# Optimization experiments

Hardware: AMD Instinct MI355X
Metric: run time of the kernel (lower is better)

## Reference

```python
import jax, jax.numpy as jnp
import numpy as np

NPAT, NCON, E, H, L = 50000, 20000, 800000, 128, 2
DP, DC = 64, 128
N = NPAT + NCON  # homogeneous node count


def setup_inputs() -> dict:
    key = jax.random.key(0)
    k = jax.random.split(key, 12)
    s = 0.05
    return {
        "x_patient": jax.random.normal(k[0], (NPAT, DP), jnp.float32),
        "x_concept": jax.random.normal(k[1], (NCON, DC), jnp.float32),
        "W_p": jax.random.normal(k[2], (DP, H), jnp.float32) * s,
        "b_p": jnp.zeros((H,), jnp.float32),
        "W_c": jax.random.normal(k[3], (DC, H), jnp.float32) * s,
        "b_c": jnp.zeros((H,), jnp.float32),
        "W_root": jax.random.normal(k[4], (L, H, H), jnp.float32) * s,
        "b_root": jnp.zeros((L, H), jnp.float32),
        "W_rel": jax.random.normal(k[5], (L, 2, H, H), jnp.float32) * s,
        "src_pc": jax.random.randint(k[6], (E,), 0, NPAT),
        "dst_pc": jax.random.randint(k[7], (E,), 0, NCON),
        "src_cp": jax.random.randint(k[8], (E,), 0, NCON),
        "dst_cp": jax.random.randint(k[9], (E,), 0, NPAT),
    }


def reference(x_patient, x_concept, W_p, b_p, W_c, b_c, W_root, b_root, W_rel,
              src_pc, dst_pc, src_cp, dst_cp):
    # per-node-type linear projection, then concat into homogeneous graph
    # (patient offset 0, concept offset NPAT)
    x = jnp.concatenate([x_patient @ W_p + b_p, x_concept @ W_c + b_c], axis=0)  # [N, H]
    rel_edges = [(src_pc, dst_pc + NPAT), (src_cp + NPAT, dst_cp)]
    ones = jnp.ones((E,), jnp.float32)
    # per-relation in-degree for mean aggregation (zero-deg nodes -> 0 output)
    counts = [jnp.maximum(jax.ops.segment_sum(ones, d, num_segments=N), 1.0)[:, None]
              for _, d in rel_edges]
    for l in range(L):
        out = x @ W_root[l] + b_root[l]  # root transform + bias
        for r, (src, dst) in enumerate(rel_edges):
            msg = x[src] @ W_rel[l, r]  # [E, H] gather + relation transform
            out = out + jax.ops.segment_sum(msg, dst, num_segments=N) / counts[r]
        x = jax.nn.relu(out)
    return x  # [N, H]; rows [0:NPAT] are patient embeddings, rest concepts
```

## Files before the change

### kernel.cpp

```cpp
#include <hip/hip_runtime.h>
#include <hip/hip_bf16.h>

#define NPAT 50000
#define NCON 20000
#define NN   70000
#define EE   800000
#define H    128

#define NCON_AL  20032
#define SEGN     (NCON_AL + NPAT)
#define NBUCK    1095
#define RELSPLIT_B 313
#define BUCKCAP  5120
#define SUBS     16
#define SUBCAP   (BUCKCAP / SUBS)
#define BPE      4096
#define NBB      ((2 * EE + BPE - 1) / BPE)
#define CAP      4096

typedef __attribute__((ext_vector_type(8))) short bf16x8;
typedef __attribute__((ext_vector_type(4))) float f32x4;

__device__ inline unsigned short f2bf(float f) {
    unsigned u = __float_as_uint(f);
    unsigned r = (u + 0x7FFFu + ((u >> 16) & 1u)) >> 16;
    return (unsigned short)r;
}
__device__ inline float bf2f_lo(unsigned v) { return __uint_as_float(v << 16); }
__device__ inline float bf2f_hi(unsigned v) { return __uint_as_float(v & 0xFFFF0000u); }

__global__ void init_gcur_kernel(int* __restrict__ gcur) {
    int j = blockIdx.x * 256 + threadIdx.x;
    if (j < NBUCK * SUBS) gcur[j] = (j >> 4) * BUCKCAP + (j & (SUBS - 1)) * SUBCAP;
}

__global__ __launch_bounds__(512) void binpack_kernel(
        const int* __restrict__ dst_pc, const int* __restrict__ src_pc,
        const int* __restrict__ dst_cp, const int* __restrict__ src_cp,
        int* __restrict__ gcur, unsigned* __restrict__ pairs) {
    __shared__ unsigned sval[BPE];
    __shared__ unsigned short sbkt[BPE];
    __shared__ int cnt[NBUCK];
    __shared__ int delta[NBUCK];
    __shared__ int partial[512];
    int t = threadIdx.x, blk = blockIdx.x;
    int base = blk * BPE;
    int n = min(BPE, 2 * EE - base);

    for (int i = t; i < NBUCK; i += 512) cnt[i] = 0;
    __syncthreads();

    unsigned pay[8];
    int bkt[8];
#pragma unroll
    for (int q = 0; q < 8; q++) {
        int li = q * 512 + t;
        bkt[q] = -1;
        if (li < n) {
            int i = base + li;
            int seg, src;
            if (i < EE) { seg = dst_pc[i];                src = src_pc[i]; }
            else        { seg = NCON_AL + dst_cp[i - EE]; src = src_cp[i - EE]; }
            int b = seg >> 6;
            pay[q] = (unsigned)src | ((unsigned)(seg & 63) << 16);
            bkt[q] = b;
            atomicAdd(&cnt[b], 1);
        }
    }
    __syncthreads();

    const int PER = (NBUCK + 511) / 512;
    int beg = t * PER;
    int s = 0;
#pragma unroll
    for (int k = 0; k < PER; k++) { int i = beg + k; if (i < NBUCK) s += cnt[i]; }
    partial[t] = s;
    __syncthreads();
    for (int o = 1; o < 512; o <<= 1) {
        int v = (t >= o) ? partial[t - o] : 0;
        __syncthreads();
        partial[t] += v;
        __syncthreads();
    }
    int run = partial[t] - s;
    int sub = blk & (SUBS - 1);
    int prefk[PER];
#pragma unroll
    for (int k = 0; k < PER; k++) {
        int i = beg + k;
        if (i < NBUCK) {
            prefk[k] = run;
            int c = cnt[i];
            if (c > 0) {
                int gb = atomicAdd(&gcur[i * SUBS + sub], c);
                delta[i] = gb - run;
            }
            run += c;
        }
    }
    __syncthreads();
#pragma unroll
    for (int k = 0; k < PER; k++) { int i = beg + k; if (i < NBUCK) cnt[i] = prefk[k]; }
    __syncthreads();

#pragma unroll
    for (int q = 0; q < 8; q++) {
        if (bkt[q] >= 0) {
            int b = bkt[q];
            int pos = atomicAdd(&cnt[b], 1);
            sval[pos] = pay[q];
            sbkt[pos] = (unsigned short)b;
        }
    }
    __syncthreads();
    for (int i = t; i < n; i += 512)
        pairs[delta[sbkt[i]] + i] = sval[i];
}

__global__ __launch_bounds__(512) void aggregate_kernel(
        const unsigned short* __restrict__ xbf, const unsigned* __restrict__ pairs,
        const int* __restrict__ gcur, unsigned short* __restrict__ aggn) {
    __shared__ int cnt64[64];
    __shared__ int soff[65];
    __shared__ int scur[64];
    __shared__ unsigned short ssrc[CAP];
    int t = threadIdx.x, b = blockIdx.x;
    if (t < 64) cnt64[t] = 0;
    __syncthreads();
    for (int s = 0; s < SUBS; s++) {
        int rbase = b * BUCKCAP + s * SUBCAP;
        int rcnt = gcur[b * SUBS + s] - rbase;
        for (int i = t; i < rcnt; i += 512)
            atomicAdd(&cnt64[pairs[rbase + i] >> 16], 1);
    }
    __syncthreads();
    if (t < 64) {
        int v = cnt64[t];
        int s = v;
#pragma unroll
        for (int o = 1; o < 64; o <<= 1) {
            int u = __shfl_up(s, o);
            if (t >= o) s += u;
        }
        soff[t + 1] = s;
        if (t == 0) soff[0] = 0;
        scur[t] = s - v;
    }
    __syncthreads();
    for (int s = 0; s < SUBS; s++) {
        int rbase = b * BUCKCAP + s * SUBCAP;
        int rcnt = gcur[b * SUBS + s] - rbase;
        for (int i = t; i < rcnt; i += 512) {
            unsigned p = pairs[rbase + i];
            int pos = atomicAdd(&scur[p >> 16], 1);
            ssrc[pos] = (unsigned short)(p & 0xFFFF);
        }
    }
    __syncthreads();
    int wv = t >> 6, lane = t & 63;
    int h = lane >> 5, cl = lane & 31;
    int rowbase = (b < RELSPLIT_B) ? 0 : NPAT;
    int seglim  = (b < RELSPLIT_B) ? NCON : SEGN;
    const unsigned* xw = (const unsigned*)xbf;
    for (int i = 0; i < 8; i++) {
        int d = wv * 8 + i;
        int seg = b * 64 + d;
        if (seg >= seglim) continue;
        int beg = soff[d], end = soff[d + 1];
        float4 a0 = {0.f, 0.f, 0.f, 0.f}, a1 = {0.f, 0.f, 0.f, 0.f};
        int j = beg;
        if ((end - beg) & 1) {
            int s0 = ssrc[j];
            uint2 v = *(const uint2*)&xw[(size_t)(rowbase + s0) * 64 + 2 * cl];
            if (h == 0) {
                a0.x += bf2f_lo(v.x); a0.y += bf2f_hi(v.x);
                a0.z += bf2f_lo(v.y); a0.w += bf2f_hi(v.y);
            }
            j++;
        }
        for (; j + 3 < end; j += 4) {
            int sA = ssrc[j + h];
            int sB = ssrc[j + 2 + h];
            uint2 vA = *(const uint2*)&xw[(size_t)(rowbase + sA) * 64 + 2 * cl];
            uint2 vB = *(const uint2*)&xw[(size_t)(rowbase + sB) * 64 + 2 * cl];
            a0.x += bf2f_lo(vA.x); a0.y += bf2f_hi(vA.x);
            a0.z += bf2f_lo(vA.y); a0.w += bf2f_hi(vA.y);
            a1.x += bf2f_lo(vB.x); a1.y += bf2f_hi(vB.x);
            a1.z += bf2f_lo(vB.y); a1.w += bf2f_hi(vB.y);
        }
        if (j + 1 < end) {
            int sA = ssrc[j + h];
            uint2 vA = *(const uint2*)&xw[(size_t)(rowbase + sA) * 64 + 2 * cl];
            a0.x += bf2f_lo(vA.x); a0.y += bf2f_hi(vA.x);
            a0.z += bf2f_lo(vA.y); a0.w += bf2f_hi(vA.y);
        }
        a0.x += a1.x; a0.y += a1.y; a0.z += a1.z; a0.w += a1.w;
        a0.x += __shfl_xor(a0.x, 32);
        a0.y += __shfl_xor(a0.y, 32);
        a0.z += __shfl_xor(a0.z, 32);
        a0.w += __shfl_xor(a0.w, 32);
        if (h == 0) {
            float inv = 1.0f / (float)max(end - beg, 1);
            ushort4 o;
            o.x = f2bf(a0.x * inv); o.y = f2bf(a0.y * inv);
            o.z = f2bf(a0.z * inv); o.w = f2bf(a0.w * inv);
            *(ushort4*)&aggn[(size_t)seg * H + 4 * cl] = o;
        }
    }
}

#define BM 128
#define BK 8

struct GemmJob {
    const float* A1;
    const float* B1;
    const float* bias; unsigned short* Cbf;
    int lda1, K1, M;
};

__global__ void gemm_dual_kernel(GemmJob j0, GemmJob j1, int nb0) {
    __shared__ float sA[BK][BM];
    __shared__ float sB[BK][H];
    bool first = (int)blockIdx.x < nb0;
    GemmJob j = first ? j0 : j1;
    int bm = (first ? blockIdx.x : blockIdx.x - nb0) * BM;
    int tid = threadIdx.x;
    int am = tid >> 1;
    int ak = (tid & 1) * 4;
    int bk = tid >> 5;
    int bn = (tid & 31) * 4;
    int ty = tid >> 4;
    int tx = tid & 15;
    float acc[8][8] = {};
    for (int k0 = 0; k0 < j.K1; k0 += BK) {
        int gm = bm + am; if (gm >= j.M) gm = j.M - 1;
        float4 av = *(const float4*)&j.A1[(size_t)gm * j.lda1 + k0 + ak];
        float4 bv = *(const float4*)&j.B1[(size_t)(k0 + bk) * H + bn];
        __syncthreads();
        sA[ak + 0][am] = av.x; sA[ak + 1][am] = av.y;
        sA[ak + 2][am] = av.z; sA[ak + 3][am] = av.w;
        *(float4*)&sB[bk][bn] = bv;
        __syncthreads();
#pragma unroll
        for (int k = 0; k < BK; k++) {
            float a[8], bb[8];
            *(float4*)&a[0] = *(const float4*)&sA[k][ty * 8];
            *(float4*)&a[4] = *(const float4*)&sA[k][ty * 8 + 4];
            *(float4*)&bb[0] = *(const float4*)&sB[k][tx * 4];
            *(float4*)&bb[4] = *(const float4*)&sB[k][64 + tx * 4];
#pragma unroll
            for (int i = 0; i < 8; i++)
#pragma unroll
                for (int jj = 0; jj < 8; jj++)
                    acc[i][jj] += a[i] * bb[jj];
        }
    }
    float bcol[8];
    *(float4*)&bcol[0] = *(const float4*)&j.bias[tx * 4];
    *(float4*)&bcol[4] = *(const float4*)&j.bias[64 + tx * 4];
#pragma unroll
    for (int i = 0; i < 8; i++) {
        int gr = bm + ty * 8 + i;
        if (gr < j.M) {
#pragma unroll
            for (int q = 0; q < 8; q++) {
                float v = acc[i][q] + bcol[q];
                int gc = (q < 4) ? (tx * 4 + q) : (64 + tx * 4 + q - 4);
                j.Cbf[(size_t)gr * H + gc] = f2bf(v);
            }
        }
    }
}

struct MJob {
    const unsigned short* A1;
    const unsigned short* A2;
    const float* B1;
    const float* B2;
    const float* bias;
    float* C;
    unsigned short* Cbf;
    int M;
};

__global__ __launch_bounds__(256) void gemm_mfma_kernel(MJob j0, MJob j1, int nb0) {
    __shared__ unsigned short sA[128][40];
    __shared__ unsigned short sBT[128][40];
    bool first = (int)blockIdx.x < nb0;
    MJob J = first ? j0 : j1;
    int bm = (first ? (int)blockIdx.x : (int)blockIdx.x - nb0) * 128;
    int tid = threadIdx.x;
    int wv = tid >> 6, lane = tid & 63;
    int wr = wv >> 1, wc = wv & 1;
    int m16 = lane & 15, kg = lane >> 4;

    f32x4 acc[4][4];
#pragma unroll
    for (int a = 0; a < 4; a++)
#pragma unroll
        for (int c = 0; c < 4; c++) acc[a][c] = (f32x4){0.f, 0.f, 0.f, 0.f};

    int ar = tid >> 1, ah = tid & 1;
    int gmA = bm + ar; if (gmA >= J.M) gmA = J.M - 1;
    int bn = tid & 127, bk0 = tid >> 7;

#pragma unroll
    for (int kt = 0; kt < 8; kt++) {
        int k0 = kt * 32;
        const unsigned short* asrc = (k0 < 128)
            ? (J.A1 + (size_t)gmA * H + k0)
            : (J.A2 + (size_t)gmA * H + (k0 - 128));
        const uint4* a4 = (const uint4*)(asrc + ah * 16);
        uint4 av0 = a4[0], av1 = a4[1];
        const float* bsrc = (k0 < 128) ? (J.B1 + (size_t)k0 * H)
                                       : (J.B2 + (size_t)(k0 - 128) * H);
        float bvals[16];
#pragma unroll
        for (int kk = 0; kk < 16; kk++) bvals[kk] = bsrc[(size_t)(2 * kk + bk0) * H + bn];
        __syncthreads();
        { uint4* d4 = (uint4*)&sA[ar][ah * 16]; d4[0] = av0; d4[1] = av1; }
#pragma unroll
        for (int kk = 0; kk < 16; kk++) sBT[bn][2 * kk + bk0] = f2bf(bvals[kk]);
        __syncthreads();
        bf16x8 af[4], bfg[4];
#pragma unroll
        for (int mt = 0; mt < 4; mt++)
            af[mt] = *(bf16x8*)&sA[wr * 64 + mt * 16 + m16][kg * 8];
#pragma unroll
        for (int nt = 0; nt < 4; nt++)
            bfg[nt] = *(bf16x8*)&sBT[wc * 64 + nt * 16 + m16][kg * 8];
#pragma unroll
        for (int mt = 0; mt < 4; mt++)
#pragma unroll
            for (int nt = 0; nt < 4; nt++)
                acc[mt][nt] = __builtin_amdgcn_mfma_f32_16x16x32_bf16(
                    af[mt], bfg[nt], acc[mt][nt], 0, 0, 0);
    }
    float bv[4];
#pragma unroll
    for (int nt = 0; nt < 4; nt++) bv[nt] = J.bias[wc * 64 + nt * 16 + m16];
#pragma unroll
    for (int mt = 0; mt < 4; mt++) {
        int gr0 = bm + wr * 64 + mt * 16 + kg * 4;
#pragma unroll
        for (int r = 0; r < 4; r++) {
            int gr = gr0 + r;
            if (gr < J.M) {
#pragma unroll
                for (int nt = 0; nt < 4; nt++) {
                    int gc = wc * 64 + nt * 16 + m16;
                    float v = fmaxf(acc[mt][nt][r] + bv[nt], 0.f);
                    if (J.C)   J.C[(size_t)gr * H + gc] = v;
                    if (J.Cbf) J.Cbf[(size_t)gr * H + gc] = f2bf(v);
                }
            }
        }
    }
}


extern "C" void kernel_launch(void* const* d_in, const int* in_sizes, int n_in,
                              void* d_out, int out_size, void* d_ws, size_t ws_size,
                              hipStream_t stream) {
    const float* x_patient = (const float*)d_in[0];
    const float* x_concept = (const float*)d_in[1];
    const float* W_p       = (const float*)d_in[2];
    const float* b_p       = (const float*)d_in[3];
    const float* W_c       = (const float*)d_in[4];
    const float* b_c       = (const float*)d_in[5];
    const float* W_root    = (const float*)d_in[6];
    const float* b_root    = (const float*)d_in[7];
    const float* W_rel     = (const float*)d_in[8];
    const int*   src_pc    = (const int*)d_in[9];
    const int*   dst_pc    = (const int*)d_in[10];
    const int*   src_cp    = (const int*)d_in[11];
    const int*   dst_cp    = (const int*)d_in[12];
    float* out = (float*)d_out;

    char* w = (char*)d_ws;
    unsigned short* xbf  = (unsigned short*)w; w += (size_t)NN * H * 2;
    unsigned short* aggn = (unsigned short*)w; w += (size_t)SEGN * H * 2;
    int* gcur = (int*)w;            w += (size_t)NBUCK * SUBS * 4;
    unsigned* pairs = (unsigned*)w; w += (size_t)NBUCK * BUCKCAP * 4;

    init_gcur_kernel<<<(NBUCK * SUBS + 255) / 256, 256, 0, stream>>>(gcur);
    binpack_kernel<<<NBB, 512, 0, stream>>>(dst_pc, src_pc, dst_cp, src_cp, gcur, pairs);

    const int PB = (NPAT + BM - 1) / BM;
    const int CB = (NCON + BM - 1) / BM;

    {
        GemmJob jp = { x_patient, W_p, b_p, xbf, 64, 64, NPAT };
        GemmJob jc = { x_concept, W_c, b_c, xbf + (size_t)NPAT * H, 128, 128, NCON };
        gemm_dual_kernel<<<PB + CB, 256, 0, stream>>>(jp, jc, PB);
    }

    for (int l = 0; l < 2; l++) {
        aggregate_kernel<<<NBUCK, 512, 0, stream>>>(xbf, pairs, gcur, aggn);
        const float* Wroot_l = W_root + (size_t)l * H * H;
        const float* Wrel_l0 = W_rel + (size_t)(l * 2 + 0) * H * H;
        const float* Wrel_l1 = W_rel + (size_t)(l * 2 + 1) * H * H;
        const float* br = b_root + (size_t)l * H;
        float* cp = (l == 1) ? out : nullptr;
        float* cc = (l == 1) ? out + (size_t)NPAT * H : nullptr;
        unsigned short* bp = (l == 0) ? xbf : nullptr;
        unsigned short* bc = (l == 0) ? xbf + (size_t)NPAT * H : nullptr;
        MJob jp = { xbf, aggn + (size_t)NCON_AL * H, Wroot_l, Wrel_l1, br,
                    cp, bp, NPAT };
        MJob jc = { xbf + (size_t)NPAT * H, aggn, Wroot_l, Wrel_l0, br,
                    cc, bc, NCON };
        gemm_mfma_kernel<<<PB + CB, 256, 0, stream>>>(jp, jc, PB);
    }
}
```

Measured before the change: 331.8 us.

## Fuse neighbor aggregation with root/relation MFMA GEMM per 64-row bucket

```diff
diff --git a/kernel.cpp b/kernel.cpp
--- a/kernel.cpp
+++ b/kernel.cpp
@@ -17,6 +17,7 @@
 #define BPE      4096
 #define NBB      ((2 * EE + BPE - 1) / BPE)
 #define CAP      4096
+#define STR      136
 
 typedef __attribute__((ext_vector_type(8))) short bf16x8;
 typedef __attribute__((ext_vector_type(4))) float f32x4;
@@ -117,16 +118,43 @@
         pairs[delta[sbkt[i]] + i] = sval[i];
 }
 
-__global__ __launch_bounds__(512) void aggregate_kernel(
-        const unsigned short* __restrict__ xbf, const unsigned* __restrict__ pairs,
-        const int* __restrict__ gcur, unsigned short* __restrict__ aggn) {
+__global__ __launch_bounds__(512) void layer_fused_kernel(
+        const unsigned short* __restrict__ xin,
+        const unsigned* __restrict__ pairs,
+        const int* __restrict__ gcur,
+        const float* __restrict__ Wroot,
+        const float* __restrict__ WrelC,
+        const float* __restrict__ WrelP,
+        const float* __restrict__ bias,
+        float* __restrict__ Cout,
+        unsigned short* __restrict__ Cbf) {
+    __shared__ unsigned short ssrc[CAP];
+    __shared__ unsigned short sX[64][STR];
+    __shared__ unsigned short sAgg[64][STR];
+    __shared__ unsigned short sBT[128][40];
     __shared__ int cnt64[64];
     __shared__ int soff[65];
     __shared__ int scur[64];
-    __shared__ unsigned short ssrc[CAP];
+
     int t = threadIdx.x, b = blockIdx.x;
+    bool isCon = (b < RELSPLIT_B);
+    int wv = t >> 6, lane = t & 63;
+
+    int row0 = isCon ? (NPAT + b * 64) : ((b - RELSPLIT_B) * 64);
+    int rowclamp = (isCon ? NN : NPAT) - 1;
+    {
+#pragma unroll
+        for (int e = 0; e < 2; e++) {
+            int idx = t * 2 + e;
+            int r = idx >> 4, q = idx & 15;
+            int gr = min(row0 + r, rowclamp);
+            uint4 v = *(const uint4*)&xin[(size_t)gr * H + q * 8];
+            *(uint4*)&sX[r][q * 8] = v;
+        }
+    }
     if (t < 64) cnt64[t] = 0;
     __syncthreads();
+
     for (int s = 0; s < SUBS; s++) {
         int rbase = b * BUCKCAP + s * SUBCAP;
         int rcnt = gcur[b * SUBS + s] - rbase;
@@ -157,21 +185,18 @@
         }
     }
     __syncthreads();
-    int wv = t >> 6, lane = t & 63;
+
     int h = lane >> 5, cl = lane & 31;
-    int rowbase = (b < RELSPLIT_B) ? 0 : NPAT;
-    int seglim  = (b < RELSPLIT_B) ? NCON : SEGN;
-    const unsigned* xw = (const unsigned*)xbf;
+    int srcbase = isCon ? 0 : NPAT;
+    const unsigned* xw = (const unsigned*)xin;
     for (int i = 0; i < 8; i++) {
         int d = wv * 8 + i;
-        int seg = b * 64 + d;
-        if (seg >= seglim) continue;
         int beg = soff[d], end = soff[d + 1];
         float4 a0 = {0.f, 0.f, 0.f, 0.f}, a1 = {0.f, 0.f, 0.f, 0.f};
         int j = beg;
         if ((end - beg) & 1) {
             int s0 = ssrc[j];
-            uint2 v = *(const uint2*)&xw[(size_t)(rowbase + s0) * 64 + 2 * cl];
+            uint2 v = *(const uint2*)&xw[(size_t)(srcbase + s0) * 64 + 2 * cl];
             if (h == 0) {
                 a0.x += bf2f_lo(v.x); a0.y += bf2f_hi(v.x);
                 a0.z += bf2f_lo(v.y); a0.w += bf2f_hi(v.y);
@@ -181,8 +206,8 @@
         for (; j + 3 < end; j += 4) {
             int sA = ssrc[j + h];
             int sB = ssrc[j + 2 + h];
-            uint2 vA = *(const uint2*)&xw[(size_t)(rowbase + sA) * 64 + 2 * cl];
-            uint2 vB = *(const uint2*)&xw[(size_t)(rowbase + sB) * 64 + 2 * cl];
+            uint2 vA = *(const uint2*)&xw[(size_t)(srcbase + sA) * 64 + 2 * cl];
+            uint2 vB = *(const uint2*)&xw[(size_t)(srcbase + sB) * 64 + 2 * cl];
             a0.x += bf2f_lo(vA.x); a0.y += bf2f_hi(vA.x);
             a0.z += bf2f_lo(vA.y); a0.w += bf2f_hi(vA.y);
             a1.x += bf2f_lo(vB.x); a1.y += bf2f_hi(vB.x);
@@ -190,7 +215,7 @@
         }
         if (j + 1 < end) {
             int sA = ssrc[j + h];
-            uint2 vA = *(const uint2*)&xw[(size_t)(rowbase + sA) * 64 + 2 * cl];
+            uint2 vA = *(const uint2*)&xw[(size_t)(srcbase + sA) * 64 + 2 * cl];
             a0.x += bf2f_lo(vA.x); a0.y += bf2f_hi(vA.x);
             a0.z += bf2f_lo(vA.y); a0.w += bf2f_hi(vA.y);
         }
@@ -204,7 +229,54 @@
             ushort4 o;
             o.x = f2bf(a0.x * inv); o.y = f2bf(a0.y * inv);
             o.z = f2bf(a0.z * inv); o.w = f2bf(a0.w * inv);
-            *(ushort4*)&aggn[(size_t)seg * H + 4 * cl] = o;
+            *(ushort4*)&sAgg[d][4 * cl] = o;
+        }
+    }
+
+    const float* W2 = isCon ? WrelC : WrelP;
+    int m16 = lane & 15, kg = lane >> 4;
+    f32x4 acc[4];
+#pragma unroll
+    for (int mt = 0; mt < 4; mt++) acc[mt] = (f32x4){0.f, 0.f, 0.f, 0.f};
+    int bn = t & 127, kq = t >> 7;
+
+#pragma unroll
+    for (int kt = 0; kt < 8; kt++) {
+        int k0 = (kt & 3) * 32;
+        const float* bsrc = ((kt < 4) ? Wroot : W2) + (size_t)k0 * H;
+        float bvals[8];
+#pragma unroll
+        for (int kk = 0; kk < 8; kk++) bvals[kk] = bsrc[(size_t)(kk * 4 + kq) * H + bn];
+        __syncthreads();
+#pragma unroll
+        for (int kk = 0; kk < 8; kk++) sBT[bn][kk * 4 + kq] = f2bf(bvals[kk]);
+        __syncthreads();
+        const unsigned short (*Asrc)[STR] = (kt < 4) ? sX : sAgg;
+        bf16x8 bfg = *(bf16x8*)&sBT[wv * 16 + m16][kg * 8];
+        bf16x8 af[4];
+#pragma unroll
+        for (int mt = 0; mt < 4; mt++)
+            af[mt] = *(bf16x8*)&Asrc[mt * 16 + m16][k0 + kg * 8];
+#pragma unroll
+        for (int mt = 0; mt < 4; mt++)
+            acc[mt] = __builtin_amdgcn_mfma_f32_16x16x32_bf16(af[mt], bfg, acc[mt], 0, 0, 0);
+    }
+
+    float bv = bias[wv * 16 + m16];
+    int lim = isCon ? NCON : NPAT;
+    int lbase = isCon ? b * 64 : (b - RELSPLIT_B) * 64;
+#pragma unroll
+    for (int mt = 0; mt < 4; mt++) {
+#pragma unroll
+        for (int r = 0; r < 4; r++) {
+            int lr = mt * 16 + kg * 4 + r;
+            if (lbase + lr < lim) {
+                int grow = row0 + lr;
+                int gcol = wv * 16 + m16;
+                float v = fmaxf(acc[mt][r] + bv, 0.f);
+                if (Cout) Cout[(size_t)grow * H + gcol] = v;
+                if (Cbf)  Cbf[(size_t)grow * H + gcol] = f2bf(v);
+            }
         }
     }
 }
@@ -273,92 +345,6 @@
     }
 }
 
-struct MJob {
-    const unsigned short* A1;
-    const unsigned short* A2;
-    const float* B1;
-    const float* B2;
-    const float* bias;
-    float* C;
-    unsigned short* Cbf;
-    int M;
-};
-
-__global__ __launch_bounds__(256) void gemm_mfma_kernel(MJob j0, MJob j1, int nb0) {
-    __shared__ unsigned short sA[128][40];
-    __shared__ unsigned short sBT[128][40];
-    bool first = (int)blockIdx.x < nb0;
-    MJob J = first ? j0 : j1;
-    int bm = (first ? (int)blockIdx.x : (int)blockIdx.x - nb0) * 128;
-    int tid = threadIdx.x;
-    int wv = tid >> 6, lane = tid & 63;
-    int wr = wv >> 1, wc = wv & 1;
-    int m16 = lane & 15, kg = lane >> 4;
-
-    f32x4 acc[4][4];
-#pragma unroll
-    for (int a = 0; a < 4; a++)
-#pragma unroll
-        for (int c = 0; c < 4; c++) acc[a][c] = (f32x4){0.f, 0.f, 0.f, 0.f};
-
-    int ar = tid >> 1, ah = tid & 1;
-    int gmA = bm + ar; if (gmA >= J.M) gmA = J.M - 1;
-    int bn = tid & 127, bk0 = tid >> 7;
-
-#pragma unroll
-    for (int kt = 0; kt < 8; kt++) {
-        int k0 = kt * 32;
-        const unsigned short* asrc = (k0 < 128)
-            ? (J.A1 + (size_t)gmA * H + k0)
-            : (J.A2 + (size_t)gmA * H + (k0 - 128));
-        const uint4* a4 = (const uint4*)(asrc + ah * 16);
-        uint4 av0 = a4[0], av1 = a4[1];
-        const float* bsrc = (k0 < 128) ? (J.B1 + (size_t)k0 * H)
-                                       : (J.B2 + (size_t)(k0 - 128) * H);
-        float bvals[16];
-#pragma unroll
-        for (int kk = 0; kk < 16; kk++) bvals[kk] = bsrc[(size_t)(2 * kk + bk0) * H + bn];
-        __syncthreads();
-        { uint4* d4 = (uint4*)&sA[ar][ah * 16]; d4[0] = av0; d4[1] = av1; }
-#pragma unroll
-        for (int kk = 0; kk < 16; kk++) sBT[bn][2 * kk + bk0] = f2bf(bvals[kk]);
-        __syncthreads();
-        bf16x8 af[4], bfg[4];
-#pragma unroll
-        for (int mt = 0; mt < 4; mt++)
-            af[mt] = *(bf16x8*)&sA[wr * 64 + mt * 16 + m16][kg * 8];
-#pragma unroll
-        for (int nt = 0; nt < 4; nt++)
-            bfg[nt] = *(bf16x8*)&sBT[wc * 64 + nt * 16 + m16][kg * 8];
-#pragma unroll
-        for (int mt = 0; mt < 4; mt++)
-#pragma unroll
-            for (int nt = 0; nt < 4; nt++)
-                acc[mt][nt] = __builtin_amdgcn_mfma_f32_16x16x32_bf16(
-                    af[mt], bfg[nt], acc[mt][nt], 0, 0, 0);
-    }
-    float bv[4];
-#pragma unroll
-    for (int nt = 0; nt < 4; nt++) bv[nt] = J.bias[wc * 64 + nt * 16 + m16];
-#pragma unroll
-    for (int mt = 0; mt < 4; mt++) {
-        int gr0 = bm + wr * 64 + mt * 16 + kg * 4;
-#pragma unroll
-        for (int r = 0; r < 4; r++) {
-            int gr = gr0 + r;
-            if (gr < J.M) {
-#pragma unroll
-                for (int nt = 0; nt < 4; nt++) {
-                    int gc = wc * 64 + nt * 16 + m16;
-                    float v = fmaxf(acc[mt][nt][r] + bv[nt], 0.f);
-                    if (J.C)   J.C[(size_t)gr * H + gc] = v;
-                    if (J.Cbf) J.Cbf[(size_t)gr * H + gc] = f2bf(v);
-                }
-            }
-        }
-    }
-}
-
 
 extern "C" void kernel_launch(void* const* d_in, const int* in_sizes, int n_in,
                               void* d_out, int out_size, void* d_ws, size_t ws_size,
@@ -379,8 +365,8 @@
     float* out = (float*)d_out;
 
     char* w = (char*)d_ws;
-    unsigned short* xbf  = (unsigned short*)w; w += (size_t)NN * H * 2;
-    unsigned short* aggn = (unsigned short*)w; w += (size_t)SEGN * H * 2;
+    unsigned short* xbf0 = (unsigned short*)w; w += (size_t)NN * H * 2;
+    unsigned short* xbf1 = (unsigned short*)w; w += (size_t)NN * H * 2;
     int* gcur = (int*)w;            w += (size_t)NBUCK * SUBS * 4;
     unsigned* pairs = (unsigned*)w; w += (size_t)NBUCK * BUCKCAP * 4;
 
@@ -391,25 +377,20 @@
     const int CB = (NCON + BM - 1) / BM;
 
     {
-        GemmJob jp = { x_patient, W_p, b_p, xbf, 64, 64, NPAT };
-        GemmJob jc = { x_concept, W_c, b_c, xbf + (size_t)NPAT * H, 128, 128, NCON };
+        GemmJob jp = { x_patient, W_p, b_p, xbf0, 64, 64, NPAT };
+        GemmJob jc = { x_concept, W_c, b_c, xbf0 + (size_t)NPAT * H, 128, 128, NCON };
         gemm_dual_kernel<<<PB + CB, 256, 0, stream>>>(jp, jc, PB);
     }
 
     for (int l = 0; l < 2; l++) {
-        aggregate_kernel<<<NBUCK, 512, 0, stream>>>(xbf, pairs, gcur, aggn);
+        const unsigned short* xin = (l == 0) ? xbf0 : xbf1;
         const float* Wroot_l = W_root + (size_t)l * H * H;
         const float* Wrel_l0 = W_rel + (size_t)(l * 2 + 0) * H * H;
         const float* Wrel_l1 = W_rel + (size_t)(l * 2 + 1) * H * H;
         const float* br = b_root + (size_t)l * H;
-        float* cp = (l == 1) ? out : nullptr;
-        float* cc = (l == 1) ? out + (size_t)NPAT * H : nullptr;
-        unsigned short* bp = (l == 0) ? xbf : nullptr;
-        unsigned short* bc = (l == 0) ? xbf + (size_t)NPAT * H : nullptr;
-        MJob jp = { xbf, aggn + (size_t)NCON_AL * H, Wroot_l, Wrel_l1, br,
-                    cp, bp, NPAT };
-        MJob jc = { xbf + (size_t)NPAT * H, aggn, Wroot_l, Wrel_l0, br,
-                    cc, bc, NCON };
-        gemm_mfma_kernel<<<PB + CB, 256, 0, stream>>>(jp, jc, PB);
-    }
-}
+        float* cOut = (l == 1) ? out : nullptr;
+        unsigned short* cBf = (l == 0) ? xbf1 : nullptr;
+        layer_fused_kernel<<<NBUCK, 512, 0, stream>>>(
+            xin, pairs, gcur, Wroot_l, Wrel_l0, Wrel_l1, br, cOut, cBf);
+    }
+}
```

Result: slower. 376.9 us (+13.6%).

## Pre-transpose weights to bf16 once and use LDS-free per-wave MFMA GEMMs

Applied to the files above, without the earlier changes.

```diff
diff --git a/kernel.cpp b/kernel.cpp
--- a/kernel.cpp
+++ b/kernel.cpp
@@ -18,6 +18,17 @@
 #define NBB      ((2 * EE + BPE - 1) / BPE)
 #define CAP      4096
 
+#define PSTRIPS  1563
+#define CSTRIPS  625
+#define TSTRIPS  (PSTRIPS + CSTRIPS)
+#define GBLK     ((TSTRIPS + 3) / 4)
+
+#define WPT_OFF    0
+#define WCT_OFF    8192
+#define WROOTT_OFF 24576
+#define WRELT_OFF  57344
+#define WBFT_SHORTS 122880
+
 typedef __attribute__((ext_vector_type(8))) short bf16x8;
 typedef __attribute__((ext_vector_type(4))) float f32x4;
 
@@ -29,9 +40,34 @@
 __device__ inline float bf2f_lo(unsigned v) { return __uint_as_float(v << 16); }
 __device__ inline float bf2f_hi(unsigned v) { return __uint_as_float(v & 0xFFFF0000u); }
 
-__global__ void init_gcur_kernel(int* __restrict__ gcur) {
-    int j = blockIdx.x * 256 + threadIdx.x;
-    if (j < NBUCK * SUBS) gcur[j] = (j >> 4) * BUCKCAP + (j & (SUBS - 1)) * SUBCAP;
+__global__ __launch_bounds__(256) void prep_kernel(
+        const float* __restrict__ Wp, const float* __restrict__ Wc,
+        const float* __restrict__ Wroot, const float* __restrict__ Wrel,
+        unsigned short* __restrict__ wbfT, int* __restrict__ gcur) {
+    int b = blockIdx.x, t = threadIdx.x;
+    if (b < 69) {
+        int j = b * 256 + t;
+        if (j < NBUCK * SUBS) gcur[j] = (j >> 4) * BUCKCAP + (j & (SUBS - 1)) * SUBCAP;
+        return;
+    }
+    int wb = b - 69;
+    const float* src; int K, outoff, eoff;
+    if (wb < 4) { src = Wp; K = 64; outoff = WPT_OFF; eoff = wb * 2048; }
+    else {
+        int m = (wb - 4) >> 3, sub = (wb - 4) & 7;
+        eoff = sub * 2048;
+        if (m == 0)      { src = Wc;                    K = 128; outoff = WCT_OFF; }
+        else if (m < 3)  { src = Wroot + (m - 1) * 16384; K = 128; outoff = WROOTT_OFF + (m - 1) * 16384; }
+        else             { src = Wrel + (m - 3) * 16384;  K = 128; outoff = WRELT_OFF + (m - 3) * 16384; }
+    }
+    int e = eoff + t * 8;
+    int k = e >> 7, n0 = e & 127;
+    float4 v0 = *(const float4*)&src[e];
+    float4 v1 = *(const float4*)&src[e + 4];
+    unsigned short o[8] = { f2bf(v0.x), f2bf(v0.y), f2bf(v0.z), f2bf(v0.w),
+                            f2bf(v1.x), f2bf(v1.y), f2bf(v1.z), f2bf(v1.w) };
+#pragma unroll
+    for (int j = 0; j < 8; j++) wbfT[outoff + (n0 + j) * K + k] = o[j];
 }
 
 __global__ __launch_bounds__(512) void binpack_kernel(
@@ -209,154 +245,136 @@
     }
 }
 
-#define BM 128
-#define BK 8
-
-struct GemmJob {
-    const float* A1;
-    const float* B1;
-    const float* bias; unsigned short* Cbf;
-    int lda1, K1, M;
-};
-
-__global__ void gemm_dual_kernel(GemmJob j0, GemmJob j1, int nb0) {
-    __shared__ float sA[BK][BM];
-    __shared__ float sB[BK][H];
-    bool first = (int)blockIdx.x < nb0;
-    GemmJob j = first ? j0 : j1;
-    int bm = (first ? blockIdx.x : blockIdx.x - nb0) * BM;
-    int tid = threadIdx.x;
-    int am = tid >> 1;
-    int ak = (tid & 1) * 4;
-    int bk = tid >> 5;
-    int bn = (tid & 31) * 4;
-    int ty = tid >> 4;
-    int tx = tid & 15;
-    float acc[8][8] = {};
-    for (int k0 = 0; k0 < j.K1; k0 += BK) {
-        int gm = bm + am; if (gm >= j.M) gm = j.M - 1;
-        float4 av = *(const float4*)&j.A1[(size_t)gm * j.lda1 + k0 + ak];
-        float4 bv = *(const float4*)&j.B1[(size_t)(k0 + bk) * H + bn];
-        __syncthreads();
-        sA[ak + 0][am] = av.x; sA[ak + 1][am] = av.y;
-        sA[ak + 2][am] = av.z; sA[ak + 3][am] = av.w;
-        *(float4*)&sB[bk][bn] = bv;
-        __syncthreads();
-#pragma unroll
-        for (int k = 0; k < BK; k++) {
-            float a[8], bb[8];
-            *(float4*)&a[0] = *(const float4*)&sA[k][ty * 8];
-            *(float4*)&a[4] = *(const float4*)&sA[k][ty * 8 + 4];
-            *(float4*)&bb[0] = *(const float4*)&sB[k][tx * 4];
-            *(float4*)&bb[4] = *(const float4*)&sB[k][64 + tx * 4];
-#pragma unroll
-            for (int i = 0; i < 8; i++)
-#pragma unroll
-                for (int jj = 0; jj < 8; jj++)
-                    acc[i][jj] += a[i] * bb[jj];
-        }
-    }
-    float bcol[8];
-    *(float4*)&bcol[0] = *(const float4*)&j.bias[tx * 4];
-    *(float4*)&bcol[4] = *(const float4*)&j.bias[64 + tx * 4];
-#pragma unroll
-    for (int i = 0; i < 8; i++) {
-        int gr = bm + ty * 8 + i;
-        if (gr < j.M) {
-#pragma unroll
-            for (int q = 0; q < 8; q++) {
-                float v = acc[i][q] + bcol[q];
-                int gc = (q < 4) ? (tx * 4 + q) : (64 + tx * 4 + q - 4);
-                j.Cbf[(size_t)gr * H + gc] = f2bf(v);
-            }
-        }
-    }
-}
-
-struct MJob {
-    const unsigned short* A1;
-    const unsigned short* A2;
-    const float* B1;
-    const float* B2;
-    const float* bias;
-    float* C;
-    unsigned short* Cbf;
-    int M;
-};
-
-__global__ __launch_bounds__(256) void gemm_mfma_kernel(MJob j0, MJob j1, int nb0) {
-    __shared__ unsigned short sA[128][40];
-    __shared__ unsigned short sBT[128][40];
-    bool first = (int)blockIdx.x < nb0;
-    MJob J = first ? j0 : j1;
-    int bm = (first ? (int)blockIdx.x : (int)blockIdx.x - nb0) * 128;
-    int tid = threadIdx.x;
-    int wv = tid >> 6, lane = tid & 63;
-    int wr = wv >> 1, wc = wv & 1;
+__global__ __launch_bounds__(256) void proj_kernel(
+        const float* __restrict__ xp, const float* __restrict__ xc,
+        const unsigned short* __restrict__ wbfT,
+        const float* __restrict__ bp, const float* __restrict__ bc,
+        unsigned short* __restrict__ Cbf) {
+    int strip = blockIdx.x * 4 + ((int)threadIdx.x >> 6);
+    if (strip >= TSTRIPS) return;
+    int lane = threadIdx.x & 63;
     int m16 = lane & 15, kg = lane >> 4;
-
-    f32x4 acc[4][4];
-#pragma unroll
-    for (int a = 0; a < 4; a++)
-#pragma unroll
-        for (int c = 0; c < 4; c++) acc[a][c] = (f32x4){0.f, 0.f, 0.f, 0.f};
-
-    int ar = tid >> 1, ah = tid & 1;
-    int gmA = bm + ar; if (gmA >= J.M) gmA = J.M - 1;
-    int bn = tid & 127, bk0 = tid >> 7;
-
-#pragma unroll
-    for (int kt = 0; kt < 8; kt++) {
-        int k0 = kt * 32;
-        const unsigned short* asrc = (k0 < 128)
-            ? (J.A1 + (size_t)gmA * H + k0)
-            : (J.A2 + (size_t)gmA * H + (k0 - 128));
-        const uint4* a4 = (const uint4*)(asrc + ah * 16);
-        uint4 av0 = a4[0], av1 = a4[1];
-        const float* bsrc = (k0 < 128) ? (J.B1 + (size_t)k0 * H)
-                                       : (J.B2 + (size_t)(k0 - 128) * H);
-        float bvals[16];
-#pragma unroll
-        for (int kk = 0; kk < 16; kk++) bvals[kk] = bsrc[(size_t)(2 * kk + bk0) * H + bn];
-        __syncthreads();
-        { uint4* d4 = (uint4*)&sA[ar][ah * 16]; d4[0] = av0; d4[1] = av1; }
-#pragma unroll
-        for (int kk = 0; kk < 16; kk++) sBT[bn][2 * kk + bk0] = f2bf(bvals[kk]);
-        __syncthreads();
-        bf16x8 af[4], bfg[4];
-#pragma unroll
-        for (int mt = 0; mt < 4; mt++)
-            af[mt] = *(bf16x8*)&sA[wr * 64 + mt * 16 + m16][kg * 8];
-#pragma unroll
-        for (int nt = 0; nt < 4; nt++)
-            bfg[nt] = *(bf16x8*)&sBT[wc * 64 + nt * 16 + m16][kg * 8];
-#pragma unroll
-        for (int mt = 0; mt < 4; mt++)
-#pragma unroll
-            for (int nt = 0; nt < 4; nt++)
+    bool isP = strip < PSTRIPS;
+    const float* A = isP ? xp : xc;
+    int K = isP ? 64 : 128;
+    int M = isP ? NPAT : NCON;
+    int nkt = K >> 5;
+    const unsigned short* BT = wbfT + (isP ? WPT_OFF : WCT_OFF);
+    const float* bias = isP ? bp : bc;
+    int r0 = (isP ? strip : strip - PSTRIPS) * 32;
+    int outbase = isP ? 0 : NPAT;
+    int arow0 = min(r0 + m16, M - 1);
+    int arow1 = min(r0 + 16 + m16, M - 1);
+
+    f32x4 acc[2][8];
+#pragma unroll
+    for (int mt = 0; mt < 2; mt++)
+#pragma unroll
+        for (int nt = 0; nt < 8; nt++) acc[mt][nt] = (f32x4){0.f, 0.f, 0.f, 0.f};
+
+    for (int kt = 0; kt < nkt; kt++) {
+        int kk = kt * 32 + kg * 8;
+        bf16x8 af[2];
+#pragma unroll
+        for (int mt = 0; mt < 2; mt++) {
+            const float* Ar = A + (size_t)(mt ? arow1 : arow0) * K + kk;
+            float4 v0 = *(const float4*)Ar;
+            float4 v1 = *(const float4*)(Ar + 4);
+            bf16x8 a;
+            a[0] = (short)f2bf(v0.x); a[1] = (short)f2bf(v0.y);
+            a[2] = (short)f2bf(v0.z); a[3] = (short)f2bf(v0.w);
+            a[4] = (short)f2bf(v1.x); a[5] = (short)f2bf(v1.y);
+            a[6] = (short)f2bf(v1.z); a[7] = (short)f2bf(v1.w);
+            af[mt] = a;
+        }
+        bf16x8 bfg[8];
+#pragma unroll
+        for (int nt = 0; nt < 8; nt++)
+            bfg[nt] = *(const bf16x8*)&BT[(size_t)(nt * 16 + m16) * K + kk];
+#pragma unroll
+        for (int mt = 0; mt < 2; mt++)
+#pragma unroll
+            for (int nt = 0; nt < 8; nt++)
                 acc[mt][nt] = __builtin_amdgcn_mfma_f32_16x16x32_bf16(
                     af[mt], bfg[nt], acc[mt][nt], 0, 0, 0);
     }
-    float bv[4];
-#pragma unroll
-    for (int nt = 0; nt < 4; nt++) bv[nt] = J.bias[wc * 64 + nt * 16 + m16];
-#pragma unroll
-    for (int mt = 0; mt < 4; mt++) {
-        int gr0 = bm + wr * 64 + mt * 16 + kg * 4;
+    float bv[8];
+#pragma unroll
+    for (int nt = 0; nt < 8; nt++) bv[nt] = bias[nt * 16 + m16];
+#pragma unroll
+    for (int mt = 0; mt < 2; mt++)
 #pragma unroll
         for (int r = 0; r < 4; r++) {
-            int gr = gr0 + r;
-            if (gr < J.M) {
-#pragma unroll
-                for (int nt = 0; nt < 4; nt++) {
-                    int gc = wc * 64 + nt * 16 + m16;
+            int lr = r0 + mt * 16 + kg * 4 + r;
+            if (lr < M) {
+                size_t orow = (size_t)(outbase + lr);
+#pragma unroll
+                for (int nt = 0; nt < 8; nt++)
+                    Cbf[orow * H + nt * 16 + m16] = f2bf(acc[mt][nt][r] + bv[nt]);
+            }
+        }
+}
+
+__global__ __launch_bounds__(256) void layer_kernel(
+        const unsigned short* __restrict__ xin, const unsigned short* __restrict__ aggn,
+        const unsigned short* __restrict__ wbfT, int l, const float* __restrict__ bias,
+        float* __restrict__ Cout, unsigned short* __restrict__ Cbf) {
+    int strip = blockIdx.x * 4 + ((int)threadIdx.x >> 6);
+    if (strip >= TSTRIPS) return;
+    int lane = threadIdx.x & 63;
+    int m16 = lane & 15, kg = lane >> 4;
+    bool isP = strip < PSTRIPS;
+    int M = isP ? NPAT : NCON;
+    int r0 = (isP ? strip : strip - PSTRIPS) * 32;
+    const unsigned short* A1 = xin + (size_t)(isP ? 0 : NPAT) * H;
+    const unsigned short* A2 = aggn + (size_t)(isP ? NCON_AL : 0) * H;
+    const unsigned short* BrootT = wbfT + WROOTT_OFF + l * 16384;
+    const unsigned short* BrelT  = wbfT + WRELT_OFF + (l * 2 + (isP ? 1 : 0)) * 16384;
+    int arow0 = min(r0 + m16, M - 1);
+    int arow1 = min(r0 + 16 + m16, M - 1);
+
+    f32x4 acc[2][8];
+#pragma unroll
+    for (int mt = 0; mt < 2; mt++)
+#pragma unroll
+        for (int nt = 0; nt < 8; nt++) acc[mt][nt] = (f32x4){0.f, 0.f, 0.f, 0.f};
+
+#pragma unroll
+    for (int kt = 0; kt < 8; kt++) {
+        int kk = (kt & 3) * 32 + kg * 8;
+        const unsigned short* Ab = (kt < 4) ? A1 : A2;
+        const unsigned short* Bb = (kt < 4) ? BrootT : BrelT;
+        bf16x8 af0 = *(const bf16x8*)&Ab[(size_t)arow0 * H + kk];
+        bf16x8 af1 = *(const bf16x8*)&Ab[(size_t)arow1 * H + kk];
+        bf16x8 bfg[8];
+#pragma unroll
+        for (int nt = 0; nt < 8; nt++)
+            bfg[nt] = *(const bf16x8*)&Bb[(size_t)(nt * 16 + m16) * 128 + kk];
+#pragma unroll
+        for (int nt = 0; nt < 8; nt++) {
+            acc[0][nt] = __builtin_amdgcn_mfma_f32_16x16x32_bf16(af0, bfg[nt], acc[0][nt], 0, 0, 0);
+            acc[1][nt] = __builtin_amdgcn_mfma_f32_16x16x32_bf16(af1, bfg[nt], acc[1][nt], 0, 0, 0);
+        }
+    }
+    float bv[8];
+#pragma unroll
+    for (int nt = 0; nt < 8; nt++) bv[nt] = bias[nt * 16 + m16];
+    int outbase = isP ? 0 : NPAT;
+#pragma unroll
+    for (int mt = 0; mt < 2; mt++)
+#pragma unroll
+        for (int r = 0; r < 4; r++) {
+            int lr = r0 + mt * 16 + kg * 4 + r;
+            if (lr < M) {
+                size_t orow = (size_t)(outbase + lr);
+#pragma unroll
+                for (int nt = 0; nt < 8; nt++) {
                     float v = fmaxf(acc[mt][nt][r] + bv[nt], 0.f);
-                    if (J.C)   J.C[(size_t)gr * H + gc] = v;
-                    if (J.Cbf) J.Cbf[(size_t)gr * H + gc] = f2bf(v);
+                    if (Cout) Cout[orow * H + nt * 16 + m16] = v;
+                    if (Cbf)  Cbf[orow * H + nt * 16 + m16] = f2bf(v);
                 }
             }
         }
-    }
 }
 
 
@@ -379,37 +397,22 @@
     float* out = (float*)d_out;
 
     char* w = (char*)d_ws;
-    unsigned short* xbf  = (unsigned short*)w; w += (size_t)NN * H * 2;
+    unsigned short* xbf0 = (unsigned short*)w; w += (size_t)NN * H * 2;
+    unsigned short* xbf1 = (unsigned short*)w; w += (size_t)NN * H * 2;
     unsigned short* aggn = (unsigned short*)w; w += (size_t)SEGN * H * 2;
+    unsigned short* wbfT = (unsigned short*)w; w += (size_t)WBFT_SHORTS * 2;
     int* gcur = (int*)w;            w += (size_t)NBUCK * SUBS * 4;
     unsigned* pairs = (unsigned*)w; w += (size_t)NBUCK * BUCKCAP * 4;
 
-    init_gcur_kernel<<<(NBUCK * SUBS + 255) / 256, 256, 0, stream>>>(gcur);
+    prep_kernel<<<129, 256, 0, stream>>>(W_p, W_c, W_root, W_rel, wbfT, gcur);
+    proj_kernel<<<GBLK, 256, 0, stream>>>(x_patient, x_concept, wbfT, b_p, b_c, xbf0);
     binpack_kernel<<<NBB, 512, 0, stream>>>(dst_pc, src_pc, dst_cp, src_cp, gcur, pairs);
-
-    const int PB = (NPAT + BM - 1) / BM;
-    const int CB = (NCON + BM - 1) / BM;
-
-    {
-        GemmJob jp = { x_patient, W_p, b_p, xbf, 64, 64, NPAT };
-        GemmJob jc = { x_concept, W_c, b_c, xbf + (size_t)NPAT * H, 128, 128, NCON };
-        gemm_dual_kernel<<<PB + CB, 256, 0, stream>>>(jp, jc, PB);
-    }
-
     for (int l = 0; l < 2; l++) {
-        aggregate_kernel<<<NBUCK, 512, 0, stream>>>(xbf, pairs, gcur, aggn);
-        const float* Wroot_l = W_root + (size_t)l * H * H;
-        const float* Wrel_l0 = W_rel + (size_t)(l * 2 + 0) * H * H;
-        const float* Wrel_l1 = W_rel + (size_t)(l * 2 + 1) * H * H;
-        const float* br = b_root + (size_t)l * H;
-        float* cp = (l == 1) ? out : nullptr;
-        float* cc = (l == 1) ? out + (size_t)NPAT * H : nullptr;
-        unsigned short* bp = (l == 0) ? xbf : nullptr;
-        unsigned short* bc = (l == 0) ? xbf + (size_t)NPAT * H : nullptr;
-        MJob jp = { xbf, aggn + (size_t)NCON_AL * H, Wroot_l, Wrel_l1, br,
-                    cp, bp, NPAT };
-        MJob jc = { xbf + (size_t)NPAT * H, aggn, Wroot_l, Wrel_l0, br,
-                    cc, bc, NCON };
-        gemm_mfma_kernel<<<PB + CB, 256, 0, stream>>>(jp, jc, PB);
-    }
-}
+        const unsigned short* xin = (l == 0) ? xbf0 : xbf1;
+        aggregate_kernel<<<NBUCK, 512, 0, stream>>>(xin, pairs, gcur, aggn);
+        float* cOut = (l == 1) ? out : nullptr;
+        unsigned short* cBf = (l == 0) ? xbf1 : nullptr;
+        layer_kernel<<<GBLK, 256, 0, stream>>>(xin, aggn, wbfT, l,
+                                               b_root + (size_t)l * H, cOut, cBf);
+    }
+}
```

Result: slower. 350.4 us (+5.6%).
